# Kernel tuning notes

Measured on AMD Instinct MI355X. Metric: run time of the kernel, lower is better.

## Reference

```python
import jax, jax.numpy as jnp
import numpy as np
from jax.scipy.linalg import solve_triangular

B, T, D = 2, 8192, 1024
HEAD_DIM = 128
H = D // HEAD_DIM  # 8 heads
C = 64             # chunk size (hard-coded in the torch module)


def setup_inputs() -> dict:
    key = jax.random.key(0)
    k0, k1, k2, k3 = jax.random.split(key, 4)
    scale = 0.02
    return {
        "out": jax.random.normal(k0, (B, T, D), jnp.float32),
        "W_write": jax.random.normal(k1, (D, D), jnp.float32) * scale,   # proj_write.weight (out,in)
        "W_read": jax.random.normal(k2, (D, D), jnp.float32) * scale,    # proj_read.weight
        "W_beta": jax.random.normal(k3, (H, D), jnp.float32) * scale,    # proj_beta.weight
        "decay": jnp.full((H,), 4.6, jnp.float32),                        # decay parameter
    }


def reference(out, W_write, W_read, W_beta, decay):
    Bs, Ts, Ds = out.shape
    d = HEAD_DIM
    Hn = Ds // d
    x = out.astype(jnp.float32)

    # keys: L2-normalized per head (F.normalize, eps=1e-12)
    k = x.reshape(Bs, Ts, Hn, d)
    k = k / jnp.maximum(jnp.linalg.norm(k, axis=-1, keepdims=True), 1e-12)
    k = k.transpose(0, 2, 1, 3)                                   # (B,H,T,d)
    v = (x @ W_write.T).reshape(Bs, Ts, Hn, d).transpose(0, 2, 1, 3)
    beta = jax.nn.sigmoid(x @ W_beta.T).transpose(0, 2, 1)[..., None]  # (B,H,T,1)
    v = v * beta
    k_beta = k * beta

    pad = (-Ts) % C
    if pad:
        pw = ((0, 0), (0, 0), (0, pad), (0, 0))
        k, v, k_beta = (jnp.pad(a, pw) for a in (k, v, k_beta))
    Tp = k.shape[2]
    N = Tp // C

    log_gamma = jnp.log(jax.nn.sigmoid(decay))                     # (H,)
    pos = jnp.arange(C, dtype=jnp.float32)
    cum_decay = (pos + 1.0)[None, :] * log_gamma[:, None]          # (H,C)
    Ldiff = cum_decay[:, :, None] - cum_decay[:, None, :]
    L = jnp.tril(jnp.exp(jnp.tril(Ldiff)))                         # (H,C,C)
    decay_exp = jnp.exp(cum_decay)[None, :, None, :, None]         # (1,H,1,C,1)
    chunk_total_decay = jnp.exp(cum_decay[:, -1])[None, :, None, None]  # (1,H,1,1)
    dw = jnp.exp(cum_decay[:, -1:] - cum_decay)[None, :, :, None]  # (1,H,C,1)
    de = jnp.exp(cum_decay)[None, :, :, None]                      # (1,H,C,1)

    k = k.reshape(Bs, Hn, N, C, d)
    v = v.reshape(Bs, Hn, N, C, d)
    k_beta = k_beta.reshape(Bs, Hn, N, C, d)

    # UT transform: original loop computes A = (I - A0)^{-1} with A0 strictly lower
    A0 = jnp.tril(-(jnp.einsum('bhnid,bhnjd->bhnij', k_beta, k) * L[None, :, None]), -1)
    eye = jnp.eye(C, dtype=jnp.float32)
    M = eye - A0                                                    # unit-diag lower triangular
    A = solve_triangular(M, jnp.broadcast_to(eye, M.shape), lower=True, unit_diagonal=True)

    v = A @ v
    k_cumdecay = A @ (k_beta * decay_exp)

    # inter-chunk sequential recurrence over N chunks
    kc = k.transpose(2, 0, 1, 3, 4)            # (N,B,H,C,d)
    vc = v.transpose(2, 0, 1, 3, 4)
    kcd = k_cumdecay.transpose(2, 0, 1, 3, 4)

    def step(S, inp):
        k_i, v_i, kcd_i = inp                  # (B,H,C,d)
        attn = jnp.tril(jnp.einsum('bhid,bhjd->bhij', k_i, k_i) * L[None])
        v_new = v_i - kcd_i @ S
        o_i = (k_i * de) @ S + attn @ v_new
        S_new = chunk_total_decay * S + jnp.einsum('bhcd,bhce->bhde', k_i * dw, v_new)
        return S_new, o_i

    S0 = jnp.zeros((Bs, Hn, d, d), jnp.float32)
    _, o = jax.lax.scan(step, S0, (kc, vc, kcd))  # o: (N,B,H,C,d)

    o = o.transpose(1, 2, 0, 3, 4).reshape(Bs, Hn, Tp, d)
    o = o.transpose(0, 2, 1, 3).reshape(Bs, Tp, Ds)[:, :Ts]
    return out + (o @ W_read.T).astype(out.dtype)
```

## Files before the change

kernel.cpp:

```cpp
#include <hip/hip_runtime.h>
#include <stdint.h>

#define DEV static __device__ __forceinline__

typedef float          f32x4  __attribute__((ext_vector_type(4)));
typedef short          bf16x8 __attribute__((ext_vector_type(8)));
typedef unsigned short u16x4  __attribute__((ext_vector_type(4)));
typedef unsigned short u16x8  __attribute__((ext_vector_type(8)));

#define B_   2
#define T_   8192
#define D_   1024
#define H_   8
#define HD_  128
#define N_   128

DEV float dot4(const float4& a, const float4& b) {
    return a.x * b.x + a.y * b.y + a.z * b.z + a.w * b.w;
}
DEV unsigned short f2bf(float f) {
    union { float f; unsigned u; } v; v.f = f;
    unsigned r = (v.u + 0x7fffu + ((v.u >> 16) & 1u)) >> 16;
    return (unsigned short)r;
}
DEV float bf2f(unsigned short u) {
    union { unsigned u; float f; } v; v.u = ((unsigned)u) << 16;
    return v.f;
}
DEV unsigned pk2(unsigned short h, unsigned short l) {
    return (unsigned)h | ((unsigned)l << 16);
}
DEV bf16x8 mk8(unsigned a, unsigned b, unsigned c, unsigned d) {
    union { unsigned u[4]; bf16x8 v; } t;
    t.u[0] = a; t.u[1] = b; t.u[2] = c; t.u[3] = d;
    return t.v;
}
DEV void cvt4(const float4 v, u16x4* h, u16x4* l) {
    const float* p = (const float*)&v;
    #pragma unroll
    for (int i = 0; i < 4; ++i) {
        unsigned short hv = f2bf(p[i]);
        (*h)[i] = hv;
        (*l)[i] = f2bf(p[i] - bf2f(hv));
    }
}
DEV int swzu(int c, int u) { return u ^ (((c & 7) << 2) | ((c >> 3) & 3)); }

DEV float4* r512(char* base, int r, int u) {
    return (float4*)(base + (r << 9) + ((u << 4) ^ ((r & 7) << 4)));
}

__launch_bounds__(256)
__global__ void prep_kernel(const float* __restrict__ X, const float* __restrict__ Wb,
                            unsigned short* __restrict__ khi, unsigned short* __restrict__ klo,
                            float* __restrict__ beta) {
    int bt = blockIdx.x;
    int b = bt >> 13, t = bt & 8191;
    __shared__ float xrow[D_];
    const float* xp = X + (size_t)bt * D_;
    for (int i = threadIdx.x; i < D_; i += 256) xrow[i] = xp[i];
    __syncthreads();
    int w = threadIdx.x >> 6, lane = threadIdx.x & 63;
    for (int h = w; h < H_; h += 4) {
        const float* xh = xrow + h * HD_;
        float a0 = xh[lane], a1 = xh[lane + 64];
        float s = a0 * a0 + a1 * a1;
        #pragma unroll
        for (int off = 32; off > 0; off >>= 1) s += __shfl_xor(s, off);
        float rn = 1.0f / fmaxf(sqrtf(s), 1e-12f);
        const float* wbh = Wb + (size_t)h * D_;
        float bs = 0.f;
        for (int i = lane; i < D_; i += 64) bs += xrow[i] * wbh[i];
        #pragma unroll
        for (int off = 32; off > 0; off >>= 1) bs += __shfl_xor(bs, off);
        float bet = 1.0f / (1.0f + expf(-bs));
        size_t kbase = ((size_t)(b * H_ + h) * T_ + t) * HD_;
        float x0 = a0 * rn, x1 = a1 * rn;
        unsigned short h0 = f2bf(x0), h1 = f2bf(x1);
        khi[kbase + lane]      = h0;
        khi[kbase + lane + 64] = h1;
        klo[kbase + lane]      = f2bf(x0 - bf2f(h0));
        klo[kbase + lane + 64] = f2bf(x1 - bf2f(h1));
        if (lane == 0) beta[(size_t)(b * H_ + h) * T_ + t] = bet;
    }
}

__launch_bounds__(256, 2)
__global__ void vproj_kernel(const float* __restrict__ X, const float* __restrict__ W,
                             const float* __restrict__ beta, float* __restrict__ vb) {
    extern __shared__ char gs[];
    char* AH = gs;
    char* AL = gs + 16384;
    char* BH = gs + 32768;
    char* BL = gs + 49152;
    int bm = blockIdx.x, bn = blockIdx.y;
    int tid = threadIdx.x;
    int w = tid >> 6, lr = tid & 15, lk = (tid & 63) >> 4;
    int wm = w >> 1, wn = w & 1;

    f32x4 acc[4][4];
    #pragma unroll
    for (int i = 0; i < 4; ++i)
        #pragma unroll
        for (int j = 0; j < 4; ++j) acc[i][j] = (f32x4){0.f, 0.f, 0.f, 0.f};

    for (int kt = 0; kt < 16; ++kt) {
        __syncthreads();
        #pragma unroll
        for (int q = 0; q < 8; ++q) {
            int f = tid + q * 256;
            int row = f >> 4, kq = f & 15;
            float4 av = *(const float4*)(X + (size_t)(bm * 128 + row) * D_ + kt * 64 + kq * 4);
            float4 bv = *(const float4*)(W + (size_t)(bn * 128 + row) * D_ + kt * 64 + kq * 4);
            u16x4 ah, al, bh, bl;
            cvt4(av, &ah, &al);
            cvt4(bv, &bh, &bl);
            int off = row * 128 + ((((kq >> 1) ^ (row & 7))) << 4) + ((kq & 1) << 3);
            *(u16x4*)(AH + off) = ah; *(u16x4*)(AL + off) = al;
            *(u16x4*)(BH + off) = bh; *(u16x4*)(BL + off) = bl;
        }
        __syncthreads();
        #pragma unroll
        for (int ks = 0; ks < 2; ++ks) {
            bf16x8 aH[4], aL[4], bH[4], bL[4];
            #pragma unroll
            for (int mt = 0; mt < 4; ++mt) {
                int row = wm * 64 + mt * 16 + lr;
                int off = row * 128 + (((ks * 4 + lk) ^ (row & 7)) << 4);
                aH[mt] = *(const bf16x8*)(AH + off);
                aL[mt] = *(const bf16x8*)(AL + off);
            }
            #pragma unroll
            for (int nt = 0; nt < 4; ++nt) {
                int row = wn * 64 + nt * 16 + lr;
                int off = row * 128 + (((ks * 4 + lk) ^ (row & 7)) << 4);
                bH[nt] = *(const bf16x8*)(BH + off);
                bL[nt] = *(const bf16x8*)(BL + off);
            }
            #pragma unroll
            for (int mt = 0; mt < 4; ++mt)
                #pragma unroll
                for (int nt = 0; nt < 4; ++nt) {
                    acc[mt][nt] = __builtin_amdgcn_mfma_f32_16x16x32_bf16(aH[mt], bH[nt], acc[mt][nt], 0, 0, 0);
                    acc[mt][nt] = __builtin_amdgcn_mfma_f32_16x16x32_bf16(aH[mt], bL[nt], acc[mt][nt], 0, 0, 0);
                    acc[mt][nt] = __builtin_amdgcn_mfma_f32_16x16x32_bf16(aL[mt], bH[nt], acc[mt][nt], 0, 0, 0);
                }
        }
    }
    #pragma unroll
    for (int mt = 0; mt < 4; ++mt)
        #pragma unroll
        for (int r = 0; r < 4; ++r) {
            int m = bm * 128 + wm * 64 + mt * 16 + lk * 4 + r;
            int b = m >> 13, t = m & 8191;
            float bet = beta[(size_t)(b * H_ + bn) * T_ + t];
            size_t ob = ((size_t)(b * H_ + bn) * T_ + t) * HD_;
            #pragma unroll
            for (int nt = 0; nt < 4; ++nt)
                vb[ob + wn * 64 + nt * 16 + lr] = acc[mt][nt][r] * bet;
        }
}

__launch_bounds__(256, 2)
__global__ void chunk_kernel(const unsigned short* __restrict__ khi,
                             const unsigned short* __restrict__ klo,
                             float* __restrict__ vb,
                             const float* __restrict__ beta_g,
                             const float* __restrict__ decay,
                             unsigned short* __restrict__ attn_g,
                             unsigned short* __restrict__ kcdhi_g,
                             unsigned short* __restrict__ kcdlo_g) {
    extern __shared__ char cs[];
    char*  sk = cs;
    float* sa = (float*)(cs + 32768);
    float* sm = (float*)(cs + 49152);
    __shared__ float sb[64];
    __shared__ float swgt[64];

    int cid = blockIdx.x;
    int bh = cid >> 7, cn = cid & 127;
    int h = bh & 7;
    int tid = threadIdx.x;
    float dec = decay[h];
    float sg = 1.0f / (1.0f + expf(-dec));
    float lg = logf(sg);
    size_t base = (size_t)cid * 8192;

    #pragma unroll
    for (int lq = 0; lq < 4; ++lq) {
        int f = tid + lq * 256;
        int c = f >> 4, u0 = (f & 15) << 1;
        u16x8 hh = *(const u16x8*)(khi + base + (size_t)f * 8);
        u16x8 ll = *(const u16x8*)(klo + base + (size_t)f * 8);
        float4 v0 = {bf2f(hh[0]) + bf2f(ll[0]), bf2f(hh[1]) + bf2f(ll[1]),
                     bf2f(hh[2]) + bf2f(ll[2]), bf2f(hh[3]) + bf2f(ll[3])};
        float4 v1 = {bf2f(hh[4]) + bf2f(ll[4]), bf2f(hh[5]) + bf2f(ll[5]),
                     bf2f(hh[6]) + bf2f(ll[6]), bf2f(hh[7]) + bf2f(ll[7])};
        *r512(sk, c, u0)     = v0;
        *r512(sk, c, u0 + 1) = v1;
    }
    if (tid < 64) {
        float bv = beta_g[(size_t)bh * T_ + cn * 64 + tid];
        sb[tid] = bv;
        swgt[tid] = bv * expf((float)(tid + 1) * lg);
    }
    __syncthreads();

    int bi = tid >> 4, bj = tid & 15;
    float dacc[4][4] = {};
    for (int u = 0; u < 32; ++u) {
        float4 ka[4], kc[4];
        #pragma unroll
        for (int i = 0; i < 4; ++i) ka[i] = *r512(sk, bi * 4 + i, u);
        #pragma unroll
        for (int j = 0; j < 4; ++j) kc[j] = *r512(sk, bj + 16 * j, u);
        #pragma unroll
        for (int i = 0; i < 4; ++i)
            #pragma unroll
            for (int j = 0; j < 4; ++j)
                dacc[i][j] += dot4(ka[i], kc[j]);
    }
    size_t abase = (size_t)cid * 4096;
    #pragma unroll
    for (int i = 0; i < 4; ++i) {
        int gi = bi * 4 + i;
        #pragma unroll
        for (int j = 0; j < 4; ++j) {
            int gj = bj + 16 * j;
            float dv = dacc[i][j];
            float dfac = expf((float)(gi - gj) * lg);
            attn_g[abase + (size_t)gi * 64 + gj] = (gi >= gj) ? f2bf(dv * dfac) : (unsigned short)0;
            sm[gi * 64 + gj] = (gj < gi) ? sb[gi] * dv * dfac : ((gi == gj) ? 1.f : 0.f);
        }
    }
    __syncthreads();

    if (tid < 64) {
        int j = tid;
        for (int i = 0; i < j; ++i) sa[i * 64 + j] = 0.f;
        sa[j * 64 + j] = 1.f;
        for (int i = j + 1; i < 64; ++i) {
            float s = 0.f;
            for (int p = j; p < i; ++p) s += sm[i * 64 + p] * sa[p * 64 + j];
            sa[i * 64 + j] = -s;
        }
    }
    __syncthreads();

    int ti = tid >> 4, te = tid & 15;
    {
        float ko[4][8] = {};
        for (int p = 0; p < 64; ++p) {
            float w = swgt[p];
            float4 k0 = *r512(sk, p, te * 2);
            float4 k1 = *r512(sk, p, te * 2 + 1);
            float kv[8] = {k0.x, k0.y, k0.z, k0.w, k1.x, k1.y, k1.z, k1.w};
            float a0 = sa[(ti * 4 + 0) * 64 + p] * w;
            float a1 = sa[(ti * 4 + 1) * 64 + p] * w;
            float a2 = sa[(ti * 4 + 2) * 64 + p] * w;
            float a3 = sa[(ti * 4 + 3) * 64 + p] * w;
            #pragma unroll
            for (int e = 0; e < 8; ++e) {
                ko[0][e] = fmaf(a0, kv[e], ko[0][e]);
                ko[1][e] = fmaf(a1, kv[e], ko[1][e]);
                ko[2][e] = fmaf(a2, kv[e], ko[2][e]);
                ko[3][e] = fmaf(a3, kv[e], ko[3][e]);
            }
        }
        #pragma unroll
        for (int i = 0; i < 4; ++i) {
            u16x8 hh, ll;
            #pragma unroll
            for (int e = 0; e < 8; ++e) {
                float t = -ko[i][e];
                unsigned short hv = f2bf(t);
                hh[e] = hv;
                ll[e] = f2bf(t - bf2f(hv));
            }
            size_t off = base + (size_t)(ti * 4 + i) * 128 + te * 8;
            *(u16x8*)(kcdhi_g + off) = hh;
            *(u16x8*)(kcdlo_g + off) = ll;
        }
    }
    __syncthreads();

    #pragma unroll
    for (int lq = 0; lq < 8; ++lq) {
        int f = tid + lq * 256;
        int r = f >> 5, u = f & 31;
        *r512(sk, r, u) = ((const float4*)(vb + base))[f];
    }
    __syncthreads();

    {
        float vo[4][8] = {};
        for (int p = 0; p < 64; ++p) {
            float4 v0 = *r512(sk, p, te * 2);
            float4 v1 = *r512(sk, p, te * 2 + 1);
            float vv[8] = {v0.x, v0.y, v0.z, v0.w, v1.x, v1.y, v1.z, v1.w};
            float a0 = sa[(ti * 4 + 0) * 64 + p];
            float a1 = sa[(ti * 4 + 1) * 64 + p];
            float a2 = sa[(ti * 4 + 2) * 64 + p];
            float a3 = sa[(ti * 4 + 3) * 64 + p];
            #pragma unroll
            for (int e = 0; e < 8; ++e) {
                vo[0][e] = fmaf(a0, vv[e], vo[0][e]);
                vo[1][e] = fmaf(a1, vv[e], vo[1][e]);
                vo[2][e] = fmaf(a2, vv[e], vo[2][e]);
                vo[3][e] = fmaf(a3, vv[e], vo[3][e]);
            }
        }
        #pragma unroll
        for (int i = 0; i < 4; ++i) {
            float4 lo = {vo[i][0], vo[i][1], vo[i][2], vo[i][3]};
            float4 hi = {vo[i][4], vo[i][5], vo[i][6], vo[i][7]};
            size_t off = base + (size_t)(ti * 4 + i) * 128 + te * 8;
            *(float4*)(vb + off)     = lo;
            *(float4*)(vb + off + 4) = hi;
        }
    }
}

__launch_bounds__(512, 1)
__global__ void scan_kernel(const unsigned short* __restrict__ khi,
                            const unsigned short* __restrict__ klo,
                            const float* __restrict__ vpr,
                            const unsigned short* __restrict__ kcdhi,
                            const unsigned short* __restrict__ kcdlo,
                            const unsigned short* __restrict__ att,
                            const float* __restrict__ decay,
                            unsigned short* __restrict__ obuf) {
    extern __shared__ char ls[];
    char* KP = ls;
    char* SH = ls + 65536;
    char* SL = ls + 69632;
    char* VH = ls + 73728;
    char* VL = ls + 75776;
    char* WH = ls + 77824;
    char* WL = ls + 79872;

    int bid = blockIdx.x;
    int h7 = bid & 7;
    int strip = (bid >> 3) & 7;
    int bh = ((bid >> 6) << 3) + h7;
    int e0 = strip * 16;
    int tid = threadIdx.x;
    int w = tid >> 6, l = tid & 63, lr = l & 15, lk = l >> 4;
    int grp = w >> 2, cw = w & 3;
    float dec = decay[bh & 7];
    float sg = 1.0f / (1.0f + expf(-dec));
    float lg = logf(sg);
    float g64 = expf(64.f * lg);
    float dev4[4], gw4[4];
    #pragma unroll
    for (int r = 0; r < 4; ++r) {
        int c = cw * 16 + lk * 4 + r;
        dev4[r] = expf((float)(c + 1) * lg);
        gw4[r]  = expf((float)(63 - c) * lg);
    }

    f32x4 Sacc = (f32x4){0.f, 0.f, 0.f, 0.f};

    unsigned sh_[4][4], sl_[4][4];
    bf16x8 fH[4], fL[4];
    bf16x8 atA[2];
    f32x4 vnA;

    {
        size_t nb = (size_t)bh * N_ * 8192;
        size_t na = (size_t)bh * N_ * 4096;
        #pragma unroll
        for (int q = 0; q < 4; ++q) {
            int idx = tid + q * 512;
            u16x4 hh = *(const u16x4*)(khi + nb + (size_t)idx * 4);
            u16x4 ll = *(const u16x4*)(klo + nb + (size_t)idx * 4);
            #pragma unroll
            for (int j = 0; j < 4; ++j) { sh_[q][j] = hh[j]; sl_[q][j] = ll[j]; }
        }
        if (grp == 0) {
            #pragma unroll
            for (int ks = 0; ks < 4; ++ks) {
                size_t off = nb + (size_t)(cw * 16 + lr) * 128 + ks * 32 + lk * 8;
                fH[ks] = *(const bf16x8*)(kcdhi + off);
                fL[ks] = *(const bf16x8*)(kcdlo + off);
            }
            #pragma unroll
            for (int r = 0; r < 4; ++r)
                vnA[r] = vpr[nb + (size_t)(cw * 16 + lk * 4 + r) * 128 + e0 + lr];
        } else {
            #pragma unroll
            for (int ks = 0; ks < 4; ++ks) {
                size_t off = nb + (size_t)(cw * 16 + lr) * 128 + ks * 32 + lk * 8;
                fH[ks] = *(const bf16x8*)(khi + off);
                fL[ks] = *(const bf16x8*)(klo + off);
            }
            #pragma unroll
            for (int ks2 = 0; ks2 < 2; ++ks2)
                atA[ks2] = *(const bf16x8*)(att + na + (size_t)(cw * 16 + lr) * 64 + ks2 * 32 + lk * 8);
        }
        #pragma unroll
        for (int q = 0; q < 4; ++q) {
            int idx = tid + q * 512;
            int c = idx >> 5, un = idx & 31;
            uint4 pkd = {pk2((unsigned short)sh_[q][0], (unsigned short)sl_[q][0]),
                         pk2((unsigned short)sh_[q][1], (unsigned short)sl_[q][1]),
                         pk2((unsigned short)sh_[q][2], (unsigned short)sl_[q][2]),
                         pk2((unsigned short)sh_[q][3], (unsigned short)sl_[q][3])};
            *(uint4*)(KP + c * 512 + (swzu(c, un) << 4)) = pkd;
        }
    }

    for (int cn = 0; cn < N_; ++cn) {
        const char* KPc = KP + (cn & 1) * 32768;

        {
            u16x4 h4, l4;
            #pragma unroll
            for (int r = 0; r < 4; ++r) {
                unsigned short hv = f2bf(Sacc[r]);
                h4[r] = hv;
                l4[r] = f2bf(Sacc[r] - bf2f(hv));
            }
            int unit = 2 * w + (lk >> 1);
            int off = lr * 256 + ((unit ^ (lr & 7)) << 4) + ((lk & 1) << 3);
            *(u16x4*)(SH + off) = h4;
            *(u16x4*)(SL + off) = l4;
        }
        __syncthreads();

        bf16x8 BH[4], BL[4];
        #pragma unroll
        for (int ks = 0; ks < 4; ++ks) {
            int off = lr * 256 + (((ks * 4 + lk) ^ (lr & 7)) << 4);
            BH[ks] = *(const bf16x8*)(SH + off);
            BL[ks] = *(const bf16x8*)(SL + off);
        }
        f32x4 acc1, acc2;
        if (grp == 0) {
            acc1 = vnA; acc2 = (f32x4){0.f, 0.f, 0.f, 0.f};
            __builtin_amdgcn_s_setprio(1);
            #pragma unroll
            for (int ks = 0; ks < 2; ++ks) {
                acc1 = __builtin_amdgcn_mfma_f32_16x16x32_bf16(fH[ks], BH[ks], acc1, 0, 0, 0);
                acc2 = __builtin_amdgcn_mfma_f32_16x16x32_bf16(fH[ks+2], BH[ks+2], acc2, 0, 0, 0);
                acc1 = __builtin_amdgcn_mfma_f32_16x16x32_bf16(fH[ks], BL[ks], acc1, 0, 0, 0);
                acc2 = __builtin_amdgcn_mfma_f32_16x16x32_bf16(fH[ks+2], BL[ks+2], acc2, 0, 0, 0);
                acc1 = __builtin_amdgcn_mfma_f32_16x16x32_bf16(fL[ks], BH[ks], acc1, 0, 0, 0);
                acc2 = __builtin_amdgcn_mfma_f32_16x16x32_bf16(fL[ks+2], BH[ks+2], acc2, 0, 0, 0);
            }
            __builtin_amdgcn_s_setprio(0);
            u16x4 h4, l4, wh4, wl4;
            #pragma unroll
            for (int r = 0; r < 4; ++r) {
                float vv = acc1[r] + acc2[r];
                unsigned short hv = f2bf(vv);
                h4[r] = hv; l4[r] = f2bf(vv - bf2f(hv));
                float wv = vv * gw4[r];
                unsigned short wh = f2bf(wv);
                wh4[r] = wh; wl4[r] = f2bf(wv - bf2f(wh));
            }
            int cu = 2 * cw + (lk >> 1);
            int off = lr * 128 + ((cu ^ (lr & 7)) << 4) + ((lk & 1) << 3);
            *(u16x4*)(VH + off) = h4;  *(u16x4*)(VL + off) = l4;
            *(u16x4*)(WH + off) = wh4; *(u16x4*)(WL + off) = wl4;
        } else {
            acc1 = (f32x4){0.f, 0.f, 0.f, 0.f}; acc2 = acc1;
            __builtin_amdgcn_s_setprio(1);
            #pragma unroll
            for (int ks = 0; ks < 2; ++ks) {
                acc1 = __builtin_amdgcn_mfma_f32_16x16x32_bf16(fH[ks], BH[ks], acc1, 0, 0, 0);
                acc2 = __builtin_amdgcn_mfma_f32_16x16x32_bf16(fH[ks+2], BH[ks+2], acc2, 0, 0, 0);
                acc1 = __builtin_amdgcn_mfma_f32_16x16x32_bf16(fH[ks], BL[ks], acc1, 0, 0, 0);
                acc2 = __builtin_amdgcn_mfma_f32_16x16x32_bf16(fH[ks+2], BL[ks+2], acc2, 0, 0, 0);
                acc1 = __builtin_amdgcn_mfma_f32_16x16x32_bf16(fL[ks], BH[ks], acc1, 0, 0, 0);
                acc2 = __builtin_amdgcn_mfma_f32_16x16x32_bf16(fL[ks+2], BH[ks+2], acc2, 0, 0, 0);
            }
            __builtin_amdgcn_s_setprio(0);
        }
        __syncthreads();

        bf16x8 WHf[2], WLf[2];
        #pragma unroll
        for (int ks2 = 0; ks2 < 2; ++ks2) {
            int off = lr * 128 + (((ks2 * 4 + lk) ^ (lr & 7)) << 4);
            WHf[ks2] = *(const bf16x8*)(WH + off);
            WLf[ks2] = *(const bf16x8*)(WL + off);
        }
        if (grp == 1) {
            bf16x8 VHf[2], VLf[2];
            #pragma unroll
            for (int ks2 = 0; ks2 < 2; ++ks2) {
                int off = lr * 128 + (((ks2 * 4 + lk) ^ (lr & 7)) << 4);
                VHf[ks2] = *(const bf16x8*)(VH + off);
                VLf[ks2] = *(const bf16x8*)(VL + off);
            }
            f32x4 om;
            #pragma unroll
            for (int r = 0; r < 4; ++r) om[r] = (acc1[r] + acc2[r]) * dev4[r];
            #pragma unroll
            for (int ks2 = 0; ks2 < 2; ++ks2) {
                om = __builtin_amdgcn_mfma_f32_16x16x32_bf16(atA[ks2], VHf[ks2], om, 0, 0, 0);
                om = __builtin_amdgcn_mfma_f32_16x16x32_bf16(atA[ks2], VLf[ks2], om, 0, 0, 0);
            }
            size_t ob = ((size_t)bh * T_ + (size_t)cn * 64) * 128 + e0 + lr;
            #pragma unroll
            for (int r = 0; r < 4; ++r)
                obuf[ob + (size_t)(cw * 16 + lk * 4 + r) * 128] = f2bf(om[r]);
        }

        if (cn + 1 < N_) {
            size_t nb = ((size_t)bh * N_ + cn + 1) * 8192;
            size_t na = ((size_t)bh * N_ + cn + 1) * 4096;
            #pragma unroll
            for (int q = 0; q < 4; ++q) {
                int idx = tid + q * 512;
                u16x4 hh = *(const u16x4*)(khi + nb + (size_t)idx * 4);
                u16x4 ll = *(const u16x4*)(klo + nb + (size_t)idx * 4);
                #pragma unroll
                for (int j = 0; j < 4; ++j) { sh_[q][j] = hh[j]; sl_[q][j] = ll[j]; }
            }
            if (grp == 0) {
                #pragma unroll
                for (int ks = 0; ks < 4; ++ks) {
                    size_t off = nb + (size_t)(cw * 16 + lr) * 128 + ks * 32 + lk * 8;
                    fH[ks] = *(const bf16x8*)(kcdhi + off);
                    fL[ks] = *(const bf16x8*)(kcdlo + off);
                }
                #pragma unroll
                for (int r = 0; r < 4; ++r)
                    vnA[r] = vpr[nb + (size_t)(cw * 16 + lk * 4 + r) * 128 + e0 + lr];
            } else {
                #pragma unroll
                for (int ks = 0; ks < 4; ++ks) {
                    size_t off = nb + (size_t)(cw * 16 + lr) * 128 + ks * 32 + lk * 8;
                    fH[ks] = *(const bf16x8*)(khi + off);
                    fL[ks] = *(const bf16x8*)(klo + off);
                }
                #pragma unroll
                for (int ks2 = 0; ks2 < 2; ++ks2)
                    atA[ks2] = *(const bf16x8*)(att + na + (size_t)(cw * 16 + lr) * 64 + ks2 * 32 + lk * 8);
            }
        }

        {
            #pragma unroll
            for (int r = 0; r < 4; ++r) Sacc[r] *= g64;
            int dk = w * 16 + lr;
            int du = dk >> 2, db = (dk & 3) << 2;
            bf16x8 tH[2], tL[2];
            #pragma unroll
            for (int ks2 = 0; ks2 < 2; ++ks2) {
                unsigned uv[8];
                #pragma unroll
                for (int j = 0; j < 8; ++j) {
                    int c = ks2 * 32 + lk * 8 + j;
                    uv[j] = *(const unsigned*)(KPc + c * 512 + (swzu(c, du) << 4) + db);
                }
                tH[ks2] = mk8((uv[0] & 0xffffu) | (uv[1] << 16), (uv[2] & 0xffffu) | (uv[3] << 16),
                              (uv[4] & 0xffffu) | (uv[5] << 16), (uv[6] & 0xffffu) | (uv[7] << 16));
                tL[ks2] = mk8((uv[0] >> 16) | (uv[1] & 0xffff0000u), (uv[2] >> 16) | (uv[3] & 0xffff0000u),
                              (uv[4] >> 16) | (uv[5] & 0xffff0000u), (uv[6] >> 16) | (uv[7] & 0xffff0000u));
            }
            f32x4 tmp = (f32x4){0.f, 0.f, 0.f, 0.f};
            __builtin_amdgcn_s_setprio(1);
            Sacc = __builtin_amdgcn_mfma_f32_16x16x32_bf16(tH[0], WHf[0], Sacc, 0, 0, 0);
            tmp  = __builtin_amdgcn_mfma_f32_16x16x32_bf16(tH[1], WHf[1], tmp,  0, 0, 0);
            Sacc = __builtin_amdgcn_mfma_f32_16x16x32_bf16(tH[0], WLf[0], Sacc, 0, 0, 0);
            tmp  = __builtin_amdgcn_mfma_f32_16x16x32_bf16(tH[1], WLf[1], tmp,  0, 0, 0);
            Sacc = __builtin_amdgcn_mfma_f32_16x16x32_bf16(tL[0], WHf[0], Sacc, 0, 0, 0);
            tmp  = __builtin_amdgcn_mfma_f32_16x16x32_bf16(tL[1], WHf[1], tmp,  0, 0, 0);
            __builtin_amdgcn_s_setprio(0);
            #pragma unroll
            for (int r = 0; r < 4; ++r) Sacc[r] += tmp[r];
        }

        if (cn + 1 < N_) {
            char* KPn = KP + ((cn + 1) & 1) * 32768;
            #pragma unroll
            for (int q = 0; q < 4; ++q) {
                int idx = tid + q * 512;
                int c = idx >> 5, un = idx & 31;
                uint4 pkd = {pk2((unsigned short)sh_[q][0], (unsigned short)sl_[q][0]),
                             pk2((unsigned short)sh_[q][1], (unsigned short)sl_[q][1]),
                             pk2((unsigned short)sh_[q][2], (unsigned short)sl_[q][2]),
                             pk2((unsigned short)sh_[q][3], (unsigned short)sl_[q][3])};
                *(uint4*)(KPn + c * 512 + (swzu(c, un) << 4)) = pkd;
            }
        }
    }
}

__launch_bounds__(256, 2)
__global__ void final_kernel(const float* __restrict__ X, const float* __restrict__ W,
                             const unsigned short* __restrict__ OB, float* __restrict__ out) {
    extern __shared__ char gs[];
    char* AO = gs;
    char* BH = gs + 16384;
    char* BL = gs + 32768;
    int bm = blockIdx.x, bn = blockIdx.y;
    int tid = threadIdx.x;
    int w = tid >> 6, lr = tid & 15, lk = (tid & 63) >> 4;
    int wm = w >> 1, wn = w & 1;

    f32x4 acc[4][4];
    #pragma unroll
    for (int i = 0; i < 4; ++i)
        #pragma unroll
        for (int j = 0; j < 4; ++j) acc[i][j] = (f32x4){0.f, 0.f, 0.f, 0.f};

    for (int kt = 0; kt < 16; ++kt) {
        int hh = kt >> 1, e0g = (kt & 1) * 64;
        __syncthreads();
        #pragma unroll
        for (int q = 0; q < 4; ++q) {
            int f = tid + q * 256;
            int row = f >> 3, un = f & 7;
            int m = bm * 128 + row;
            int b = m >> 13, t = m & 8191;
            u16x8 av = *(const u16x8*)(OB + (((size_t)(b * H_ + hh) * T_ + t) << 7) + e0g + un * 8);
            int off = row * 128 + ((un ^ (row & 7)) << 4);
            *(u16x8*)(AO + off) = av;
        }
        #pragma unroll
        for (int q = 0; q < 8; ++q) {
            int f = tid + q * 256;
            int row = f >> 4, kq = f & 15;
            float4 bv = *(const float4*)(W + (size_t)(bn * 128 + row) * D_ + kt * 64 + kq * 4);
            u16x4 bh, bl;
            cvt4(bv, &bh, &bl);
            int off = row * 128 + ((((kq >> 1) ^ (row & 7))) << 4) + ((kq & 1) << 3);
            *(u16x4*)(BH + off) = bh; *(u16x4*)(BL + off) = bl;
        }
        __syncthreads();
        #pragma unroll
        for (int ks = 0; ks < 2; ++ks) {
            bf16x8 aO[4], bH[4], bL[4];
            #pragma unroll
            for (int mt = 0; mt < 4; ++mt) {
                int row = wm * 64 + mt * 16 + lr;
                int off = row * 128 + (((ks * 4 + lk) ^ (row & 7)) << 4);
                aO[mt] = *(const bf16x8*)(AO + off);
            }
            #pragma unroll
            for (int nt = 0; nt < 4; ++nt) {
                int row = wn * 64 + nt * 16 + lr;
                int off = row * 128 + (((ks * 4 + lk) ^ (row & 7)) << 4);
                bH[nt] = *(const bf16x8*)(BH + off);
                bL[nt] = *(const bf16x8*)(BL + off);
            }
            #pragma unroll
            for (int mt = 0; mt < 4; ++mt)
                #pragma unroll
                for (int nt = 0; nt < 4; ++nt) {
                    acc[mt][nt] = __builtin_amdgcn_mfma_f32_16x16x32_bf16(aO[mt], bH[nt], acc[mt][nt], 0, 0, 0);
                    acc[mt][nt] = __builtin_amdgcn_mfma_f32_16x16x32_bf16(aO[mt], bL[nt], acc[mt][nt], 0, 0, 0);
                }
        }
    }
    #pragma unroll
    for (int mt = 0; mt < 4; ++mt)
        #pragma unroll
        for (int r = 0; r < 4; ++r) {
            int m = bm * 128 + wm * 64 + mt * 16 + lk * 4 + r;
            size_t xo = (size_t)m * D_ + bn * 128;
            #pragma unroll
            for (int nt = 0; nt < 4; ++nt) {
                int n = wn * 64 + nt * 16 + lr;
                out[xo + n] = X[xo + n] + acc[mt][nt][r];
            }
        }
}

extern "C" void kernel_launch(void* const* d_in, const int* in_sizes, int n_in,
                              void* d_out, int out_size, void* d_ws, size_t ws_size,
                              hipStream_t stream) {
    const float* X   = (const float*)d_in[0];
    const float* Ww  = (const float*)d_in[1];
    const float* Wr  = (const float*)d_in[2];
    const float* Wb  = (const float*)d_in[3];
    const float* dec = (const float*)d_in[4];

    char* ws = (char*)d_ws;
    unsigned short* khi  = (unsigned short*)(ws);
    unsigned short* klo  = (unsigned short*)(ws + 33554432);
    float*          vb   = (float*)(ws + 67108864);
    unsigned short* kcdh = (unsigned short*)(ws + 134217728);
    unsigned short* kcdl = (unsigned short*)(ws + 167772160);
    unsigned short* attn = (unsigned short*)(ws + 201326592);
    float*          beta = (float*)(ws + 218103808);
    unsigned short* obuf = (unsigned short*)(ws + 218628096);
    if (ws_size < 252182528ull) return;

    hipFuncSetAttribute((const void*)vproj_kernel, hipFuncAttributeMaxDynamicSharedMemorySize, 65536);
    hipFuncSetAttribute((const void*)chunk_kernel, hipFuncAttributeMaxDynamicSharedMemorySize, 65536);
    hipFuncSetAttribute((const void*)scan_kernel,  hipFuncAttributeMaxDynamicSharedMemorySize, 81920);
    hipFuncSetAttribute((const void*)final_kernel, hipFuncAttributeMaxDynamicSharedMemorySize, 49152);

    hipLaunchKernelGGL(prep_kernel, dim3(B_ * T_), dim3(256), 0, stream, X, Wb, khi, klo, beta);
    hipLaunchKernelGGL(vproj_kernel, dim3(128, 8), dim3(256), 65536, stream, X, Ww, beta, vb);
    hipLaunchKernelGGL(chunk_kernel, dim3(B_ * H_ * N_), dim3(256), 65536, stream,
                       khi, klo, vb, beta, dec, attn, kcdh, kcdl);
    hipLaunchKernelGGL(scan_kernel, dim3(128), dim3(512), 81920, stream,
                       khi, klo, vb, kcdh, kcdl, attn, dec, obuf);
    hipLaunchKernelGGL(final_kernel, dim3(128, 8), dim3(256), 49152, stream, X, Wr, obuf, (float*)d_out);
}
```

Before: 1.152 ms.

## Restructure scan kernel to single-wave blocks with precomputed transposed keys

The chunk kernel now also writes a transposed hi/lo bf16 copy of each chunk's keys. The scan kernel drops from 512 threads to one 64-thread wave per block, which removes all block-level barriers inside the sequential recurrence. That single wave now does all the work per chunk: v_new, the output, and the state update, reading operands straight from global memory instead of staging keys in LDS. The output is written back into the v buffer in fp32, and the final projection splits it into hi/lo bf16 on the fly. This trades barrier and LDS-staging overhead for far less parallelism per block, serial global loads on the critical path, and an extra MFMA pass in the final GEMM.

```diff
diff --git a/kernel.cpp b/kernel.cpp
--- a/kernel.cpp
+++ b/kernel.cpp
@@ -27,14 +27,6 @@
     union { unsigned u; float f; } v; v.u = ((unsigned)u) << 16;
     return v.f;
 }
-DEV unsigned pk2(unsigned short h, unsigned short l) {
-    return (unsigned)h | ((unsigned)l << 16);
-}
-DEV bf16x8 mk8(unsigned a, unsigned b, unsigned c, unsigned d) {
-    union { unsigned u[4]; bf16x8 v; } t;
-    t.u[0] = a; t.u[1] = b; t.u[2] = c; t.u[3] = d;
-    return t.v;
-}
 DEV void cvt4(const float4 v, u16x4* h, u16x4* l) {
     const float* p = (const float*)&v;
     #pragma unroll
@@ -44,10 +36,11 @@
         (*l)[i] = f2bf(p[i] - bf2f(hv));
     }
 }
-DEV int swzu(int c, int u) { return u ^ (((c & 7) << 2) | ((c >> 3) & 3)); }
-
 DEV float4* r512(char* base, int r, int u) {
     return (float4*)(base + (r << 9) + ((u << 4) ^ ((r & 7) << 4)));
+}
+DEV float ld_sk(char* base, int c, int dk) {
+    return *(float*)(base + (c << 9) + ((((dk >> 2) << 4) ^ ((c & 7) << 4)) + ((dk & 3) << 2)));
 }
 
 __launch_bounds__(256)
@@ -169,7 +162,9 @@
                              const float* __restrict__ decay,
                              unsigned short* __restrict__ attn_g,
                              unsigned short* __restrict__ kcdhi_g,
-                             unsigned short* __restrict__ kcdlo_g) {
+                             unsigned short* __restrict__ kcdlo_g,
+                             unsigned short* __restrict__ kThi_g,
+                             unsigned short* __restrict__ kTlo_g) {
     extern __shared__ char cs[];
     char*  sk = cs;
     float* sa = (float*)(cs + 32768);
@@ -282,6 +277,24 @@
             *(u16x8*)(kcdlo_g + off) = ll;
         }
     }
+
+    {
+        int dk = tid >> 1, ch = (tid & 1) * 32;
+        #pragma unroll
+        for (int q = 0; q < 4; ++q) {
+            u16x8 th, tl;
+            #pragma unroll
+            for (int j = 0; j < 8; ++j) {
+                float kv = ld_sk(sk, ch + q * 8 + j, dk);
+                unsigned short hv = f2bf(kv);
+                th[j] = hv;
+                tl[j] = f2bf(kv - bf2f(hv));
+            }
+            size_t off = base + (size_t)dk * 64 + ch + q * 8;
+            *(u16x8*)(kThi_g + off) = th;
+            if (kTlo_g) *(u16x8*)(kTlo_g + off) = tl;
+        }
+    }
     __syncthreads();
 
     #pragma unroll
@@ -321,282 +334,198 @@
     }
 }
 
-__launch_bounds__(512, 1)
+__launch_bounds__(64, 1)
 __global__ void scan_kernel(const unsigned short* __restrict__ khi,
                             const unsigned short* __restrict__ klo,
-                            const float* __restrict__ vpr,
-                            const unsigned short* __restrict__ kcdhi,
-                            const unsigned short* __restrict__ kcdlo,
+                            float* __restrict__ vb,
+                            const unsigned short* __restrict__ kcdh,
+                            const unsigned short* __restrict__ kcdl,
                             const unsigned short* __restrict__ att,
-                            const float* __restrict__ decay,
-                            unsigned short* __restrict__ obuf) {
-    extern __shared__ char ls[];
-    char* KP = ls;
-    char* SH = ls + 65536;
-    char* SL = ls + 69632;
-    char* VH = ls + 73728;
-    char* VL = ls + 75776;
-    char* WH = ls + 77824;
-    char* WL = ls + 79872;
+                            const unsigned short* __restrict__ kThi,
+                            const unsigned short* __restrict__ kTlo,
+                            const float* __restrict__ decay) {
+    __shared__ char SH[4096];
+    __shared__ char SL[4096];
+    __shared__ char VH[2048];
+    __shared__ char VL[2048];
+    __shared__ char WH[2048];
+    __shared__ char WL[2048];
 
     int bid = blockIdx.x;
-    int h7 = bid & 7;
+    int bh = ((bid >> 6) << 3) + (bid & 7);
     int strip = (bid >> 3) & 7;
-    int bh = ((bid >> 6) << 3) + h7;
     int e0 = strip * 16;
-    int tid = threadIdx.x;
-    int w = tid >> 6, l = tid & 63, lr = l & 15, lk = l >> 4;
-    int grp = w >> 2, cw = w & 3;
+    int l = threadIdx.x & 63;
+    int lr = l & 15, lk = l >> 4;
     float dec = decay[bh & 7];
     float sg = 1.0f / (1.0f + expf(-dec));
     float lg = logf(sg);
     float g64 = expf(64.f * lg);
-    float dev4[4], gw4[4];
-    #pragma unroll
-    for (int r = 0; r < 4; ++r) {
-        int c = cw * 16 + lk * 4 + r;
-        dev4[r] = expf((float)(c + 1) * lg);
-        gw4[r]  = expf((float)(63 - c) * lg);
-    }
-
-    f32x4 Sacc = (f32x4){0.f, 0.f, 0.f, 0.f};
-
-    unsigned sh_[4][4], sl_[4][4];
-    bf16x8 fH[4], fL[4];
-    bf16x8 atA[2];
-    f32x4 vnA;
-
-    {
-        size_t nb = (size_t)bh * N_ * 8192;
-        size_t na = (size_t)bh * N_ * 4096;
-        #pragma unroll
-        for (int q = 0; q < 4; ++q) {
-            int idx = tid + q * 512;
-            u16x4 hh = *(const u16x4*)(khi + nb + (size_t)idx * 4);
-            u16x4 ll = *(const u16x4*)(klo + nb + (size_t)idx * 4);
-            #pragma unroll
-            for (int j = 0; j < 4; ++j) { sh_[q][j] = hh[j]; sl_[q][j] = ll[j]; }
-        }
-        if (grp == 0) {
-            #pragma unroll
-            for (int ks = 0; ks < 4; ++ks) {
-                size_t off = nb + (size_t)(cw * 16 + lr) * 128 + ks * 32 + lk * 8;
-                fH[ks] = *(const bf16x8*)(kcdhi + off);
-                fL[ks] = *(const bf16x8*)(kcdlo + off);
-            }
-            #pragma unroll
-            for (int r = 0; r < 4; ++r)
-                vnA[r] = vpr[nb + (size_t)(cw * 16 + lk * 4 + r) * 128 + e0 + lr];
-        } else {
-            #pragma unroll
-            for (int ks = 0; ks < 4; ++ks) {
-                size_t off = nb + (size_t)(cw * 16 + lr) * 128 + ks * 32 + lk * 8;
-                fH[ks] = *(const bf16x8*)(khi + off);
-                fL[ks] = *(const bf16x8*)(klo + off);
-            }
-            #pragma unroll
-            for (int ks2 = 0; ks2 < 2; ++ks2)
-                atA[ks2] = *(const bf16x8*)(att + na + (size_t)(cw * 16 + lr) * 64 + ks2 * 32 + lk * 8);
-        }
-        #pragma unroll
-        for (int q = 0; q < 4; ++q) {
-            int idx = tid + q * 512;
-            int c = idx >> 5, un = idx & 31;
-            uint4 pkd = {pk2((unsigned short)sh_[q][0], (unsigned short)sl_[q][0]),
-                         pk2((unsigned short)sh_[q][1], (unsigned short)sl_[q][1]),
-                         pk2((unsigned short)sh_[q][2], (unsigned short)sl_[q][2]),
-                         pk2((unsigned short)sh_[q][3], (unsigned short)sl_[q][3])};
-            *(uint4*)(KP + c * 512 + (swzu(c, un) << 4)) = pkd;
-        }
-    }
+    float devv[4][4], gww[4][4];
+    #pragma unroll
+    for (int ct = 0; ct < 4; ++ct)
+        #pragma unroll
+        for (int r = 0; r < 4; ++r) {
+            int c = ct * 16 + lk * 4 + r;
+            devv[ct][r] = expf((float)(c + 1) * lg);
+            gww[ct][r]  = expf((float)(63 - c) * lg);
+        }
+    const bool haveLo = (kTlo != nullptr);
+
+    f32x4 Sacc[8];
+    #pragma unroll
+    for (int dt = 0; dt < 8; ++dt) Sacc[dt] = (f32x4){0.f, 0.f, 0.f, 0.f};
 
     for (int cn = 0; cn < N_; ++cn) {
-        const char* KPc = KP + (cn & 1) * 32768;
-
-        {
+        size_t cid = (size_t)bh * N_ + cn;
+        size_t cb8 = cid * 8192, cb4 = cid * 4096;
+
+        #pragma unroll
+        for (int dt = 0; dt < 8; ++dt) {
             u16x4 h4, l4;
             #pragma unroll
             for (int r = 0; r < 4; ++r) {
-                unsigned short hv = f2bf(Sacc[r]);
+                unsigned short hv = f2bf(Sacc[dt][r]);
                 h4[r] = hv;
-                l4[r] = f2bf(Sacc[r] - bf2f(hv));
-            }
-            int unit = 2 * w + (lk >> 1);
+                l4[r] = f2bf(Sacc[dt][r] - bf2f(hv));
+            }
+            int unit = 2 * dt + (lk >> 1);
             int off = lr * 256 + ((unit ^ (lr & 7)) << 4) + ((lk & 1) << 3);
             *(u16x4*)(SH + off) = h4;
             *(u16x4*)(SL + off) = l4;
         }
-        __syncthreads();
-
         bf16x8 BH[4], BL[4];
         #pragma unroll
-        for (int ks = 0; ks < 4; ++ks) {
-            int off = lr * 256 + (((ks * 4 + lk) ^ (lr & 7)) << 4);
-            BH[ks] = *(const bf16x8*)(SH + off);
-            BL[ks] = *(const bf16x8*)(SL + off);
-        }
-        f32x4 acc1, acc2;
-        if (grp == 0) {
-            acc1 = vnA; acc2 = (f32x4){0.f, 0.f, 0.f, 0.f};
-            __builtin_amdgcn_s_setprio(1);
+        for (int s = 0; s < 4; ++s) {
+            int off = lr * 256 + (((s * 4 + lk) ^ (lr & 7)) << 4);
+            BH[s] = *(const bf16x8*)(SH + off);
+            BL[s] = *(const bf16x8*)(SL + off);
+        }
+
+        #pragma unroll
+        for (int ct = 0; ct < 4; ++ct) {
+            bf16x8 cdH[4], cdL[4];
+            #pragma unroll
+            for (int ks = 0; ks < 4; ++ks) {
+                size_t off = cb8 + (size_t)(ct * 16 + lr) * 128 + ks * 32 + lk * 8;
+                cdH[ks] = *(const bf16x8*)(kcdh + off);
+                cdL[ks] = *(const bf16x8*)(kcdl + off);
+            }
+            f32x4 vn, vn2 = (f32x4){0.f, 0.f, 0.f, 0.f};
+            #pragma unroll
+            for (int r = 0; r < 4; ++r)
+                vn[r] = vb[cb8 + (size_t)(ct * 16 + lk * 4 + r) * 128 + e0 + lr];
             #pragma unroll
             for (int ks = 0; ks < 2; ++ks) {
-                acc1 = __builtin_amdgcn_mfma_f32_16x16x32_bf16(fH[ks], BH[ks], acc1, 0, 0, 0);
-                acc2 = __builtin_amdgcn_mfma_f32_16x16x32_bf16(fH[ks+2], BH[ks+2], acc2, 0, 0, 0);
-                acc1 = __builtin_amdgcn_mfma_f32_16x16x32_bf16(fH[ks], BL[ks], acc1, 0, 0, 0);
-                acc2 = __builtin_amdgcn_mfma_f32_16x16x32_bf16(fH[ks+2], BL[ks+2], acc2, 0, 0, 0);
-                acc1 = __builtin_amdgcn_mfma_f32_16x16x32_bf16(fL[ks], BH[ks], acc1, 0, 0, 0);
-                acc2 = __builtin_amdgcn_mfma_f32_16x16x32_bf16(fL[ks+2], BH[ks+2], acc2, 0, 0, 0);
-            }
-            __builtin_amdgcn_s_setprio(0);
+                vn  = __builtin_amdgcn_mfma_f32_16x16x32_bf16(cdH[ks],   BH[ks],   vn,  0, 0, 0);
+                vn2 = __builtin_amdgcn_mfma_f32_16x16x32_bf16(cdH[ks+2], BH[ks+2], vn2, 0, 0, 0);
+                vn  = __builtin_amdgcn_mfma_f32_16x16x32_bf16(cdH[ks],   BL[ks],   vn,  0, 0, 0);
+                vn2 = __builtin_amdgcn_mfma_f32_16x16x32_bf16(cdH[ks+2], BL[ks+2], vn2, 0, 0, 0);
+                vn  = __builtin_amdgcn_mfma_f32_16x16x32_bf16(cdL[ks],   BH[ks],   vn,  0, 0, 0);
+                vn2 = __builtin_amdgcn_mfma_f32_16x16x32_bf16(cdL[ks+2], BH[ks+2], vn2, 0, 0, 0);
+            }
             u16x4 h4, l4, wh4, wl4;
             #pragma unroll
             for (int r = 0; r < 4; ++r) {
-                float vv = acc1[r] + acc2[r];
+                float vv = vn[r] + vn2[r];
                 unsigned short hv = f2bf(vv);
                 h4[r] = hv; l4[r] = f2bf(vv - bf2f(hv));
-                float wv = vv * gw4[r];
+                float wv = vv * gww[ct][r];
                 unsigned short wh = f2bf(wv);
                 wh4[r] = wh; wl4[r] = f2bf(wv - bf2f(wh));
             }
-            int cu = 2 * cw + (lk >> 1);
+            int cu = 2 * ct + (lk >> 1);
             int off = lr * 128 + ((cu ^ (lr & 7)) << 4) + ((lk & 1) << 3);
             *(u16x4*)(VH + off) = h4;  *(u16x4*)(VL + off) = l4;
             *(u16x4*)(WH + off) = wh4; *(u16x4*)(WL + off) = wl4;
-        } else {
-            acc1 = (f32x4){0.f, 0.f, 0.f, 0.f}; acc2 = acc1;
-            __builtin_amdgcn_s_setprio(1);
+        }
+        bf16x8 VHf[2], VLf[2], WHf[2], WLf[2];
+        #pragma unroll
+        for (int s2 = 0; s2 < 2; ++s2) {
+            int off = lr * 128 + (((s2 * 4 + lk) ^ (lr & 7)) << 4);
+            VHf[s2] = *(const bf16x8*)(VH + off);
+            VLf[s2] = *(const bf16x8*)(VL + off);
+            WHf[s2] = *(const bf16x8*)(WH + off);
+            WLf[s2] = *(const bf16x8*)(WL + off);
+        }
+
+        #pragma unroll
+        for (int ct = 0; ct < 4; ++ct) {
+            bf16x8 kH[4], kL[4], atA[2];
+            #pragma unroll
+            for (int ks = 0; ks < 4; ++ks) {
+                size_t off = cb8 + (size_t)(ct * 16 + lr) * 128 + ks * 32 + lk * 8;
+                kH[ks] = *(const bf16x8*)(khi + off);
+                kL[ks] = *(const bf16x8*)(klo + off);
+            }
+            #pragma unroll
+            for (int s2 = 0; s2 < 2; ++s2)
+                atA[s2] = *(const bf16x8*)(att + cb4 + (size_t)(ct * 16 + lr) * 64 + s2 * 32 + lk * 8);
+            f32x4 oa = (f32x4){0.f, 0.f, 0.f, 0.f}, ob = oa;
             #pragma unroll
             for (int ks = 0; ks < 2; ++ks) {
-                acc1 = __builtin_amdgcn_mfma_f32_16x16x32_bf16(fH[ks], BH[ks], acc1, 0, 0, 0);
-                acc2 = __builtin_amdgcn_mfma_f32_16x16x32_bf16(fH[ks+2], BH[ks+2], acc2, 0, 0, 0);
-                acc1 = __builtin_amdgcn_mfma_f32_16x16x32_bf16(fH[ks], BL[ks], acc1, 0, 0, 0);
-                acc2 = __builtin_amdgcn_mfma_f32_16x16x32_bf16(fH[ks+2], BL[ks+2], acc2, 0, 0, 0);
-                acc1 = __builtin_amdgcn_mfma_f32_16x16x32_bf16(fL[ks], BH[ks], acc1, 0, 0, 0);
-                acc2 = __builtin_amdgcn_mfma_f32_16x16x32_bf16(fL[ks+2], BH[ks+2], acc2, 0, 0, 0);
-            }
-            __builtin_amdgcn_s_setprio(0);
-        }
-        __syncthreads();
-
-        bf16x8 WHf[2], WLf[2];
-        #pragma unroll
-        for (int ks2 = 0; ks2 < 2; ++ks2) {
-            int off = lr * 128 + (((ks2 * 4 + lk) ^ (lr & 7)) << 4);
-            WHf[ks2] = *(const bf16x8*)(WH + off);
-            WLf[ks2] = *(const bf16x8*)(WL + off);
-        }
-        if (grp == 1) {
-            bf16x8 VHf[2], VLf[2];
-            #pragma unroll
-            for (int ks2 = 0; ks2 < 2; ++ks2) {
-                int off = lr * 128 + (((ks2 * 4 + lk) ^ (lr & 7)) << 4);
-                VHf[ks2] = *(const bf16x8*)(VH + off);
-                VLf[ks2] = *(const bf16x8*)(VL + off);
+                oa = __builtin_amdgcn_mfma_f32_16x16x32_bf16(kH[ks],   BH[ks],   oa, 0, 0, 0);
+                ob = __builtin_amdgcn_mfma_f32_16x16x32_bf16(kH[ks+2], BH[ks+2], ob, 0, 0, 0);
+                oa = __builtin_amdgcn_mfma_f32_16x16x32_bf16(kH[ks],   BL[ks],   oa, 0, 0, 0);
+                ob = __builtin_amdgcn_mfma_f32_16x16x32_bf16(kH[ks+2], BL[ks+2], ob, 0, 0, 0);
+                oa = __builtin_amdgcn_mfma_f32_16x16x32_bf16(kL[ks],   BH[ks],   oa, 0, 0, 0);
+                ob = __builtin_amdgcn_mfma_f32_16x16x32_bf16(kL[ks+2], BH[ks+2], ob, 0, 0, 0);
             }
             f32x4 om;
             #pragma unroll
-            for (int r = 0; r < 4; ++r) om[r] = (acc1[r] + acc2[r]) * dev4[r];
-            #pragma unroll
-            for (int ks2 = 0; ks2 < 2; ++ks2) {
-                om = __builtin_amdgcn_mfma_f32_16x16x32_bf16(atA[ks2], VHf[ks2], om, 0, 0, 0);
-                om = __builtin_amdgcn_mfma_f32_16x16x32_bf16(atA[ks2], VLf[ks2], om, 0, 0, 0);
-            }
-            size_t ob = ((size_t)bh * T_ + (size_t)cn * 64) * 128 + e0 + lr;
+            for (int r = 0; r < 4; ++r) om[r] = (oa[r] + ob[r]) * devv[ct][r];
+            #pragma unroll
+            for (int s2 = 0; s2 < 2; ++s2) {
+                om = __builtin_amdgcn_mfma_f32_16x16x32_bf16(atA[s2], VHf[s2], om, 0, 0, 0);
+                om = __builtin_amdgcn_mfma_f32_16x16x32_bf16(atA[s2], VLf[s2], om, 0, 0, 0);
+            }
             #pragma unroll
             for (int r = 0; r < 4; ++r)
-                obuf[ob + (size_t)(cw * 16 + lk * 4 + r) * 128] = f2bf(om[r]);
-        }
-
-        if (cn + 1 < N_) {
-            size_t nb = ((size_t)bh * N_ + cn + 1) * 8192;
-            size_t na = ((size_t)bh * N_ + cn + 1) * 4096;
-            #pragma unroll
-            for (int q = 0; q < 4; ++q) {
-                int idx = tid + q * 512;
-                u16x4 hh = *(const u16x4*)(khi + nb + (size_t)idx * 4);
-                u16x4 ll = *(const u16x4*)(klo + nb + (size_t)idx * 4);
-                #pragma unroll
-                for (int j = 0; j < 4; ++j) { sh_[q][j] = hh[j]; sl_[q][j] = ll[j]; }
-            }
-            if (grp == 0) {
-                #pragma unroll
-                for (int ks = 0; ks < 4; ++ks) {
-                    size_t off = nb + (size_t)(cw * 16 + lr) * 128 + ks * 32 + lk * 8;
-                    fH[ks] = *(const bf16x8*)(kcdhi + off);
-                    fL[ks] = *(const bf16x8*)(kcdlo + off);
+                vb[cb8 + (size_t)(ct * 16 + lk * 4 + r) * 128 + e0 + lr] = om[r];
+        }
+
+        #pragma unroll
+        for (int dp = 0; dp < 4; ++dp) {
+            int d0 = dp * 2, d1 = dp * 2 + 1;
+            bf16x8 t0H[2], t1H[2], t0L[2], t1L[2];
+            #pragma unroll
+            for (int s2 = 0; s2 < 2; ++s2) {
+                size_t o0 = cb8 + (size_t)(d0 * 16 + lr) * 64 + s2 * 32 + lk * 8;
+                size_t o1 = cb8 + (size_t)(d1 * 16 + lr) * 64 + s2 * 32 + lk * 8;
+                t0H[s2] = *(const bf16x8*)(kThi + o0);
+                t1H[s2] = *(const bf16x8*)(kThi + o1);
+                if (haveLo) {
+                    t0L[s2] = *(const bf16x8*)(kTlo + o0);
+                    t1L[s2] = *(const bf16x8*)(kTlo + o1);
                 }
-                #pragma unroll
-                for (int r = 0; r < 4; ++r)
-                    vnA[r] = vpr[nb + (size_t)(cw * 16 + lk * 4 + r) * 128 + e0 + lr];
-            } else {
-                #pragma unroll
-                for (int ks = 0; ks < 4; ++ks) {
-                    size_t off = nb + (size_t)(cw * 16 + lr) * 128 + ks * 32 + lk * 8;
-                    fH[ks] = *(const bf16x8*)(khi + off);
-                    fL[ks] = *(const bf16x8*)(klo + off);
+            }
+            f32x4 s0 = Sacc[d0], s1 = Sacc[d1];
+            #pragma unroll
+            for (int r = 0; r < 4; ++r) { s0[r] *= g64; s1[r] *= g64; }
+            #pragma unroll
+            for (int s2 = 0; s2 < 2; ++s2) {
+                s0 = __builtin_amdgcn_mfma_f32_16x16x32_bf16(t0H[s2], WHf[s2], s0, 0, 0, 0);
+                s1 = __builtin_amdgcn_mfma_f32_16x16x32_bf16(t1H[s2], WHf[s2], s1, 0, 0, 0);
+                s0 = __builtin_amdgcn_mfma_f32_16x16x32_bf16(t0H[s2], WLf[s2], s0, 0, 0, 0);
+                s1 = __builtin_amdgcn_mfma_f32_16x16x32_bf16(t1H[s2], WLf[s2], s1, 0, 0, 0);
+                if (haveLo) {
+                    s0 = __builtin_amdgcn_mfma_f32_16x16x32_bf16(t0L[s2], WHf[s2], s0, 0, 0, 0);
+                    s1 = __builtin_amdgcn_mfma_f32_16x16x32_bf16(t1L[s2], WHf[s2], s1, 0, 0, 0);
                 }
-                #pragma unroll
-                for (int ks2 = 0; ks2 < 2; ++ks2)
-                    atA[ks2] = *(const bf16x8*)(att + na + (size_t)(cw * 16 + lr) * 64 + ks2 * 32 + lk * 8);
-            }
-        }
-
-        {
-            #pragma unroll
-            for (int r = 0; r < 4; ++r) Sacc[r] *= g64;
-            int dk = w * 16 + lr;
-            int du = dk >> 2, db = (dk & 3) << 2;
-            bf16x8 tH[2], tL[2];
-            #pragma unroll
-            for (int ks2 = 0; ks2 < 2; ++ks2) {
-                unsigned uv[8];
-                #pragma unroll
-                for (int j = 0; j < 8; ++j) {
-                    int c = ks2 * 32 + lk * 8 + j;
-                    uv[j] = *(const unsigned*)(KPc + c * 512 + (swzu(c, du) << 4) + db);
-                }
-                tH[ks2] = mk8((uv[0] & 0xffffu) | (uv[1] << 16), (uv[2] & 0xffffu) | (uv[3] << 16),
-                              (uv[4] & 0xffffu) | (uv[5] << 16), (uv[6] & 0xffffu) | (uv[7] << 16));
-                tL[ks2] = mk8((uv[0] >> 16) | (uv[1] & 0xffff0000u), (uv[2] >> 16) | (uv[3] & 0xffff0000u),
-                              (uv[4] >> 16) | (uv[5] & 0xffff0000u), (uv[6] >> 16) | (uv[7] & 0xffff0000u));
-            }
-            f32x4 tmp = (f32x4){0.f, 0.f, 0.f, 0.f};
-            __builtin_amdgcn_s_setprio(1);
-            Sacc = __builtin_amdgcn_mfma_f32_16x16x32_bf16(tH[0], WHf[0], Sacc, 0, 0, 0);
-            tmp  = __builtin_amdgcn_mfma_f32_16x16x32_bf16(tH[1], WHf[1], tmp,  0, 0, 0);
-            Sacc = __builtin_amdgcn_mfma_f32_16x16x32_bf16(tH[0], WLf[0], Sacc, 0, 0, 0);
-            tmp  = __builtin_amdgcn_mfma_f32_16x16x32_bf16(tH[1], WLf[1], tmp,  0, 0, 0);
-            Sacc = __builtin_amdgcn_mfma_f32_16x16x32_bf16(tL[0], WHf[0], Sacc, 0, 0, 0);
-            tmp  = __builtin_amdgcn_mfma_f32_16x16x32_bf16(tL[1], WHf[1], tmp,  0, 0, 0);
-            __builtin_amdgcn_s_setprio(0);
-            #pragma unroll
-            for (int r = 0; r < 4; ++r) Sacc[r] += tmp[r];
-        }
-
-        if (cn + 1 < N_) {
-            char* KPn = KP + ((cn + 1) & 1) * 32768;
-            #pragma unroll
-            for (int q = 0; q < 4; ++q) {
-                int idx = tid + q * 512;
-                int c = idx >> 5, un = idx & 31;
-                uint4 pkd = {pk2((unsigned short)sh_[q][0], (unsigned short)sl_[q][0]),
-                             pk2((unsigned short)sh_[q][1], (unsigned short)sl_[q][1]),
-                             pk2((unsigned short)sh_[q][2], (unsigned short)sl_[q][2]),
-                             pk2((unsigned short)sh_[q][3], (unsigned short)sl_[q][3])};
-                *(uint4*)(KPn + c * 512 + (swzu(c, un) << 4)) = pkd;
-            }
+            }
+            Sacc[d0] = s0; Sacc[d1] = s1;
         }
     }
 }
 
 __launch_bounds__(256, 2)
 __global__ void final_kernel(const float* __restrict__ X, const float* __restrict__ W,
-                             const unsigned short* __restrict__ OB, float* __restrict__ out) {
+                             const float* __restrict__ OB, float* __restrict__ out) {
     extern __shared__ char gs[];
-    char* AO = gs;
-    char* BH = gs + 16384;
-    char* BL = gs + 32768;
+    char* AH = gs;
+    char* AL = gs + 16384;
+    char* BH = gs + 32768;
+    char* BL = gs + 49152;
     int bm = blockIdx.x, bn = blockIdx.y;
     int tid = threadIdx.x;
     int w = tid >> 6, lr = tid & 15, lk = (tid & 63) >> 4;
@@ -612,34 +541,30 @@
         int hh = kt >> 1, e0g = (kt & 1) * 64;
         __syncthreads();
         #pragma unroll
-        for (int q = 0; q < 4; ++q) {
-            int f = tid + q * 256;
-            int row = f >> 3, un = f & 7;
-            int m = bm * 128 + row;
-            int b = m >> 13, t = m & 8191;
-            u16x8 av = *(const u16x8*)(OB + (((size_t)(b * H_ + hh) * T_ + t) << 7) + e0g + un * 8);
-            int off = row * 128 + ((un ^ (row & 7)) << 4);
-            *(u16x8*)(AO + off) = av;
-        }
-        #pragma unroll
         for (int q = 0; q < 8; ++q) {
             int f = tid + q * 256;
             int row = f >> 4, kq = f & 15;
+            int m = bm * 128 + row;
+            int b = m >> 13, t = m & 8191;
+            float4 av = *(const float4*)(OB + (((size_t)(b * H_ + hh) * T_ + t) << 7) + e0g + kq * 4);
             float4 bv = *(const float4*)(W + (size_t)(bn * 128 + row) * D_ + kt * 64 + kq * 4);
-            u16x4 bh, bl;
+            u16x4 ah, al, bh, bl;
+            cvt4(av, &ah, &al);
             cvt4(bv, &bh, &bl);
             int off = row * 128 + ((((kq >> 1) ^ (row & 7))) << 4) + ((kq & 1) << 3);
+            *(u16x4*)(AH + off) = ah; *(u16x4*)(AL + off) = al;
             *(u16x4*)(BH + off) = bh; *(u16x4*)(BL + off) = bl;
         }
         __syncthreads();
         #pragma unroll
         for (int ks = 0; ks < 2; ++ks) {
-            bf16x8 aO[4], bH[4], bL[4];
+            bf16x8 aH[4], aL[4], bH[4], bL[4];
             #pragma unroll
             for (int mt = 0; mt < 4; ++mt) {
                 int row = wm * 64 + mt * 16 + lr;
                 int off = row * 128 + (((ks * 4 + lk) ^ (row & 7)) << 4);
-                aO[mt] = *(const bf16x8*)(AO + off);
+                aH[mt] = *(const bf16x8*)(AH + off);
+                aL[mt] = *(const bf16x8*)(AL + off);
             }
             #pragma unroll
             for (int nt = 0; nt < 4; ++nt) {
@@ -652,8 +577,9 @@
             for (int mt = 0; mt < 4; ++mt)
                 #pragma unroll
                 for (int nt = 0; nt < 4; ++nt) {
-                    acc[mt][nt] = __builtin_amdgcn_mfma_f32_16x16x32_bf16(aO[mt], bH[nt], acc[mt][nt], 0, 0, 0);
-                    acc[mt][nt] = __builtin_amdgcn_mfma_f32_16x16x32_bf16(aO[mt], bL[nt], acc[mt][nt], 0, 0, 0);
+                    acc[mt][nt] = __builtin_amdgcn_mfma_f32_16x16x32_bf16(aH[mt], bH[nt], acc[mt][nt], 0, 0, 0);
+                    acc[mt][nt] = __builtin_amdgcn_mfma_f32_16x16x32_bf16(aH[mt], bL[nt], acc[mt][nt], 0, 0, 0);
+                    acc[mt][nt] = __builtin_amdgcn_mfma_f32_16x16x32_bf16(aL[mt], bH[nt], acc[mt][nt], 0, 0, 0);
                 }
         }
     }
@@ -688,19 +614,21 @@
     unsigned short* kcdl = (unsigned short*)(ws + 167772160);
     unsigned short* attn = (unsigned short*)(ws + 201326592);
     float*          beta = (float*)(ws + 218103808);
-    unsigned short* obuf = (unsigned short*)(ws + 218628096);
+    unsigned short* kThi = (unsigned short*)(ws + 218628096);
+    unsigned short* kTlo = (ws_size >= 285736960ull)
+                         ? (unsigned short*)(ws + 252182528)
+                         : (unsigned short*)nullptr;
     if (ws_size < 252182528ull) return;
 
     hipFuncSetAttribute((const void*)vproj_kernel, hipFuncAttributeMaxDynamicSharedMemorySize, 65536);
     hipFuncSetAttribute((const void*)chunk_kernel, hipFuncAttributeMaxDynamicSharedMemorySize, 65536);
-    hipFuncSetAttribute((const void*)scan_kernel,  hipFuncAttributeMaxDynamicSharedMemorySize, 81920);
-    hipFuncSetAttribute((const void*)final_kernel, hipFuncAttributeMaxDynamicSharedMemorySize, 49152);
+    hipFuncSetAttribute((const void*)final_kernel, hipFuncAttributeMaxDynamicSharedMemorySize, 65536);
 
     hipLaunchKernelGGL(prep_kernel, dim3(B_ * T_), dim3(256), 0, stream, X, Wb, khi, klo, beta);
     hipLaunchKernelGGL(vproj_kernel, dim3(128, 8), dim3(256), 65536, stream, X, Ww, beta, vb);
     hipLaunchKernelGGL(chunk_kernel, dim3(B_ * H_ * N_), dim3(256), 65536, stream,
-                       khi, klo, vb, beta, dec, attn, kcdh, kcdl);
-    hipLaunchKernelGGL(scan_kernel, dim3(128), dim3(512), 81920, stream,
-                       khi, klo, vb, kcdh, kcdl, attn, dec, obuf);
-    hipLaunchKernelGGL(final_kernel, dim3(128, 8), dim3(256), 49152, stream, X, Wr, obuf, (float*)d_out);
-}
+                       khi, klo, vb, beta, dec, attn, kcdh, kcdl, kThi, kTlo);
+    hipLaunchKernelGGL(scan_kernel, dim3(128), dim3(64), 0, stream,
+                       khi, klo, vb, kcdh, kcdl, attn, kThi, kTlo, dec);
+    hipLaunchKernelGGL(final_kernel, dim3(128, 8), dim3(256), 65536, stream, X, Wr, vb, (float*)d_out);
+}
```

Result: slower. 3.097 ms (+168.8%).
